# Optimization experiments

Measured on AMD Instinct MI355X. Metric: run time of the kernel, lower is better.

## Reference

```python
import jax, jax.numpy as jnp
import numpy as np

D = 64; T = 128; B = 64; R = 20; SEE = 10; H = 4; C = 4
N = 300000; P = 4000; K = 256


def setup_inputs() -> dict:
    key = jax.random.key(0)
    ks = jax.random.split(key, 24)
    g = lambda k, s: jax.random.normal(k, s, dtype=jnp.float32) * 0.05
    return {
        "prob_id": jax.random.randint(ks[0], (T, B), 0, P),
        "skills": jax.random.randint(ks[1], (T, B, C), 0, K),
        "response": jax.random.randint(ks[2], (T, B), 0, 2),
        "bg_index": jax.random.randint(ks[3], (T, B, R), 0, N),
        "mem_prob_ids": jax.random.randint(ks[4], (N,), 0, P),
        "mem_resp": jax.random.randint(ks[5], (N,), 0, 2),
        "mem_concepts": jax.random.randint(ks[6], (N, C), 0, K),
        "states_mem": g(ks[7], (N, D)),
        "concept_emb": g(ks[8], (K - 1, D)),
        "prob_emb": g(ks[9], (P - 1, D)),
        "W_pred": g(ks[10], (9 * D, 1)), "b_pred": jnp.zeros((1,), jnp.float32),
        "W_ih": g(ks[11], (4 * D, 3 * D)), "W_hh": g(ks[12], (D, 3 * D)),
        "b_ih": jnp.zeros((3 * D,), jnp.float32), "b_hh": jnp.zeros((3 * D,), jnp.float32),
        "W_batch": g(ks[13], (H, 3 * D, D)), "b_batch": jnp.zeros((H, D), jnp.float32),
        "W_bg": g(ks[14], (H, 3 * D, D)), "b_bg": jnp.zeros((H, D), jnp.float32),
        "W_bgint": g(ks[15], (6 * D, 6 * D)), "b_bgint": jnp.zeros((6 * D,), jnp.float32),
        "W_hisint": g(ks[16], (2 * D, 6 * D)), "b_hisint": jnp.zeros((6 * D,), jnp.float32),
        "W_inmap": g(ks[17], (10 * D, 4 * D)), "b_inmap": jnp.zeros((4 * D,), jnp.float32),
        "dir_w": g(ks[18], (2, 1)), "heads_map": g(ks[19], (H, 1)),
    }


def _forward(floats, ints):
    (states_mem, concept_emb, prob_emb, W_pred, b_pred, W_ih, W_hh, b_ih, b_hh,
     W_batch, b_batch, W_bg, b_bg, W_bgint, b_bgint, W_hisint, b_hisint,
     W_inmap, b_inmap, dir_w, heads_map) = floats
    prob_id, skills, response, bg_index, mem_prob_ids, mem_resp, mem_concepts = ints
    f32 = states_mem.dtype
    # embedding tables with zero row 0 (padding id)
    prob_cat = jnp.concatenate([jnp.zeros((1, D), f32), prob_emb], axis=0)
    conc_cat = jnp.concatenate([jnp.zeros((1, D), f32), concept_emb], axis=0)

    def prob_rep(pid, sk):
        pr = prob_cat[pid]                                     # [..., D]
        fsum = jnp.sum((sk != 0).astype(f32), axis=-1)
        div = jnp.where(fsum == 0, 1.0, fsum)[..., None]
        mean = jnp.sum(conc_cat[sk], axis=-2) / div            # masked-mean concept emb
        return jnp.concatenate([mean, pr], axis=-1)            # [..., 2D]

    dw = jax.nn.softmax(dir_w, axis=0)                          # [2,1]
    hm = heads_map[:, 0]                                        # [H]

    def step(carry, xt):
        h, h_buf, resp_buf, v_buf, t = carry
        pid, sk, resp, bgi = xt
        respf = resp.astype(f32)
        v = prob_rep(pid, sk)                                   # [B,2D]
        hidden_v = jnp.concatenate([h, v], axis=-1)             # [B,3D]
        bgi = bgi[:, :SEE]                                      # keep first see_ref refs
        bg_h = states_mem[bgi]                                  # [B,S,D] irregular gather
        bg_v = prob_rep(mem_prob_ids[bgi], mem_concepts[bgi])   # [B,S,2D]
        bg_r = mem_resp[bgi].astype(f32)[..., None]             # [B,S,1]
        all_hv = jnp.concatenate([bg_h, bg_v], axis=-1)         # [B,S,3D]
        bg_ctx = jnp.concatenate([all_hv * bg_r, all_hv * (1.0 - bg_r)], axis=-1)  # [B,S,6D]
        # multi-head attention over retrieved background states
        q = jnp.einsum('bk,hkd->bhd', hidden_v, W_batch) + b_batch[None]
        kk = jnp.einsum('bsk,hkd->bhsd', all_hv, W_bg) + b_bg[None, :, None, :]
        att = jax.nn.softmax(jnp.einsum('bhd,bhsd->bhs', q, kk) / np.sqrt(3.0 * D), axis=-1)
        heads = jnp.einsum('bhs,bsk->bhk', att, bg_ctx)          # [B,H,6D]
        bg_atts = jnp.einsum('bhk,h->bk', heads, hm)             # [B,6D]
        # attention over own history (positions 0..t valid)
        rb = resp_buf.astype(f32)[..., None]                     # [B,T+1,1]
        hr_cat = jnp.concatenate([h_buf * rb, h_buf * (1.0 - rb)], axis=-1)  # [B,T+1,2D]
        sc = jnp.einsum('bk,btk->bt', v, v_buf) / np.sqrt(2.0 * D)
        sc = jnp.where(jnp.arange(T + 1)[None, :] <= t, sc, -1e9)
        his_atts = jnp.einsum('bt,btk->bk', jax.nn.softmax(sc, axis=-1), hr_cat)  # [B,2D]
        peer = (bg_atts @ W_bgint + b_bgint) * dw[0, 0] + (his_atts @ W_hisint + b_hisint) * dw[1, 0]
        prob = (jnp.concatenate([peer, v, h], axis=-1) @ W_pred + b_pred)[:, 0]
        v_resp = jnp.concatenate([v * respf[:, None], v * (1.0 - respf[:, None])], axis=-1)
        gru_in = jnp.concatenate([peer, v_resp], axis=-1) @ W_inmap + b_inmap  # [B,4D]
        # GRU cell (torch GRUCell convention)
        gx = gru_in @ W_ih + b_ih
        gh = h @ W_hh + b_hh
        xr, xz, xn = jnp.split(gx, 3, axis=-1)
        hr, hz, hn = jnp.split(gh, 3, axis=-1)
        r = jax.nn.sigmoid(xr + hr)
        z = jax.nn.sigmoid(xz + hz)
        n = jnp.tanh(xn + r * hn)
        new_h = (1.0 - z) * n + z * h
        h_buf = h_buf.at[:, t + 1].set(new_h)
        resp_buf = resp_buf.at[:, t + 1].set(resp.astype(resp_buf.dtype))
        v_buf = v_buf.at[:, t + 1].set(v)
        return (new_h, h_buf, resp_buf, v_buf, t + 1), prob

    init = (jnp.zeros((B, D), f32), jnp.zeros((B, T + 1, D), f32),
            jnp.zeros((B, T + 1), jnp.int32), jnp.zeros((B, T + 1, 2 * D), f32),
            jnp.int32(0))
    xs = (prob_id, skills, response.astype(jnp.int32), bg_index)
    _, probs = jax.lax.scan(step, init, xs)                      # [T,B]
    return probs.T.reshape(-1)                                   # concat over batch, seq_num=T


def reference(prob_id, skills, response, bg_index, mem_prob_ids, mem_resp, mem_concepts,
              states_mem, concept_emb, prob_emb, W_pred, b_pred, W_ih, W_hh, b_ih, b_hh,
              W_batch, b_batch, W_bg, b_bg, W_bgint, b_bgint, W_hisint, b_hisint,
              W_inmap, b_inmap, dir_w, heads_map):
    floats = (states_mem, concept_emb, prob_emb, W_pred, b_pred, W_ih, W_hh, b_ih, b_hh,
              W_batch, b_batch, W_bg, b_bg, W_bgint, b_bgint, W_hisint, b_hisint,
              W_inmap, b_inmap, dir_w, heads_map)
    ints = (prob_id, skills, response, bg_index, mem_prob_ids, mem_resp, mem_concepts)
    return _forward(floats, ints)
```

## Files before the change

kernel.cpp:

```cpp
#include <hip/hip_runtime.h>
#include <hip/hip_bf16.h>

#define TT 128
#define BB 64
#define NITEM (TT*BB*SEE)
#define SEE 10
typedef __attribute__((ext_vector_type(8))) short short8;
typedef __attribute__((ext_vector_type(4))) float floatx4;

static __device__ __forceinline__ float wave_sum(float v) {
  v += __shfl_xor(v, 32); v += __shfl_xor(v, 16); v += __shfl_xor(v, 8);
  v += __shfl_xor(v, 4);  v += __shfl_xor(v, 2);  v += __shfl_xor(v, 1);
  return v;
}
static __device__ __forceinline__ float wave_max(float v) {
  v = fmaxf(v, __shfl_xor(v, 32)); v = fmaxf(v, __shfl_xor(v, 16)); v = fmaxf(v, __shfl_xor(v, 8));
  v = fmaxf(v, __shfl_xor(v, 4));  v = fmaxf(v, __shfl_xor(v, 2));  v = fmaxf(v, __shfl_xor(v, 1));
  return v;
}
static __device__ __forceinline__ unsigned short f2bf(float x) {
  __hip_bfloat16 h = __float2bfloat16(x);
  return *reinterpret_cast<unsigned short*>(&h);
}
static __device__ __forceinline__ float bf2f(unsigned short u) {
  unsigned v = ((unsigned)u) << 16;
  return __builtin_bit_cast(float, v);
}
static __device__ __forceinline__ unsigned int pack2(float lo, float hi) {
  return (unsigned int)f2bf(lo) | ((unsigned int)f2bf(hi) << 16);
}
static __device__ __forceinline__ void ldsbar() {
  asm volatile("s_waitcnt lgkmcnt(0)" ::: "memory");
  __builtin_amdgcn_s_barrier();
  asm volatile("" ::: "memory");
}

__global__ void build_v(const int* __restrict__ prob_id, const int* __restrict__ skills,
                        const float* __restrict__ concept_emb, const float* __restrict__ prob_emb,
                        float* __restrict__ V, float* __restrict__ VT) {
  int tb = blockIdx.x; int t = tb >> 6, b = tb & 63; int d = threadIdx.x;
  int pid = prob_id[tb];
  float pr = pid ? prob_emb[(pid - 1) * 64 + d] : 0.0f;
  int cnt = 0; float sum = 0.0f;
#pragma unroll
  for (int c = 0; c < 4; ++c) {
    int sk = skills[tb * 4 + c];
    if (sk) { ++cnt; sum += concept_emb[(sk - 1) * 64 + d]; }
  }
  float mean = sum / (float)(cnt ? cnt : 1);
  V[tb * 128 + d] = mean;
  V[tb * 128 + 64 + d] = pr;
  VT[b * 16384 + d * 128 + t] = mean;
  VT[b * 16384 + (64 + d) * 128 + t] = pr;
}

__global__ __launch_bounds__(256) void gather_ahv(
    const int* __restrict__ bg_index, const int* __restrict__ mem_prob_ids,
    const int* __restrict__ mem_concepts, const float* __restrict__ states_mem,
    const float* __restrict__ concept_emb, const float* __restrict__ prob_emb,
    unsigned short* __restrict__ AHV) {
  int gid = blockIdx.x * 256 + threadIdx.x;
  int item = gid / 96, c2 = gid - 96 * item; int d = 2 * c2;
  int t = item / 640; int rem = item - t * 640; int b = rem / 10; int s = rem - b * 10;
  int g = bg_index[(t * 64 + b) * 20 + s];
  float v0, v1;
  if (d < 64) {
    float2 sv = *(const float2*)&states_mem[g * 64 + d];
    v0 = sv.x; v1 = sv.y;
  } else if (d < 128) {
    int dd = d - 64; float s0 = 0.f, s1 = 0.f; int cnt = 0;
#pragma unroll
    for (int c = 0; c < 4; ++c) {
      int sk = mem_concepts[g * 4 + c];
      if (sk) { ++cnt; float2 e = *(const float2*)&concept_emb[(sk - 1) * 64 + dd]; s0 += e.x; s1 += e.y; }
    }
    float inv = 1.0f / (float)(cnt ? cnt : 1);
    v0 = s0 * inv; v1 = s1 * inv;
  } else {
    int dd = d - 128; int pid = mem_prob_ids[g];
    if (pid) { float2 pv = *(const float2*)&prob_emb[(pid - 1) * 64 + dd]; v0 = pv.x; v1 = pv.y; }
    else { v0 = 0.f; v1 = 0.f; }
  }
  *(unsigned int*)&AHV[(size_t)item * 192 + d] = pack2(v0, v1);
}

__global__ __launch_bounds__(256) void gemm_f32(
    const float* __restrict__ A, const float* __restrict__ B, float* __restrict__ C,
    const float* __restrict__ bias, int M, int N, int K,
    int lda, int ldb, int ldc, long sA, long sB, long sC, float scale) {
  __shared__ __align__(16) float As[64 * 36];
  __shared__ __align__(16) float Bs[32 * 64];
  const float* Ab = A + (long)blockIdx.z * sA;
  const float* Bb = B + (long)blockIdx.z * sB;
  float* Cb = C + (long)blockIdx.z * sC;
  int m0 = blockIdx.y * 64, n0 = blockIdx.x * 64;
  int tid = threadIdx.x;
  int ti = tid & 15, tj = tid >> 4;
  float acc[4][4] = {};
  for (int kc = 0; kc < K; kc += 32) {
#pragma unroll
    for (int p = 0; p < 2; ++p) {
      int q = tid + 256 * p;
      int row = q >> 3, kq = q & 7;
      *(float4*)&As[row * 36 + 4 * kq] = *(const float4*)&Ab[(size_t)(m0 + row) * lda + kc + 4 * kq];
    }
#pragma unroll
    for (int p = 0; p < 2; ++p) {
      int q = tid + 256 * p;
      int k = q >> 4, nq = q & 15;
      *(float4*)&Bs[k * 64 + 4 * nq] = *(const float4*)&Bb[(size_t)(kc + k) * ldb + n0 + 4 * nq];
    }
    __syncthreads();
#pragma unroll
    for (int k4 = 0; k4 < 8; ++k4) {
      float4 av[4], bv[4];
#pragma unroll
      for (int m = 0; m < 4; ++m) av[m] = *(const float4*)&As[(ti + 16 * m) * 36 + 4 * k4];
#pragma unroll
      for (int kk = 0; kk < 4; ++kk) bv[kk] = *(const float4*)&Bs[(4 * k4 + kk) * 64 + 4 * tj];
#pragma unroll
      for (int m = 0; m < 4; ++m) {
        const float* ap = (const float*)&av[m];
#pragma unroll
        for (int kk = 0; kk < 4; ++kk) {
          float a = ap[kk];
          acc[m][0] += a * bv[kk].x; acc[m][1] += a * bv[kk].y;
          acc[m][2] += a * bv[kk].z; acc[m][3] += a * bv[kk].w;
        }
      }
    }
    __syncthreads();
  }
  float4 bq = make_float4(0.f, 0.f, 0.f, 0.f);
  if (bias) bq = *(const float4*)&bias[n0 + 4 * tj];
#pragma unroll
  for (int m = 0; m < 4; ++m) {
    int row = m0 + ti + 16 * m;
    float4 o;
    o.x = acc[m][0] * scale + bq.x; o.y = acc[m][1] * scale + bq.y;
    o.z = acc[m][2] * scale + bq.z; o.w = acc[m][3] * scale + bq.w;
    *(float4*)&Cb[(size_t)row * ldc + n0 + 4 * tj] = o;
  }
}

__global__ __launch_bounds__(256) void k_small(
    const float* __restrict__ W_batch, const float* __restrict__ W_bg, const float* __restrict__ b_bg,
    const float* __restrict__ W_bgint, const float* __restrict__ b_bgint,
    const float* __restrict__ W_hisint, const float* __restrict__ b_hisint,
    const float* __restrict__ W_ih, const float* __restrict__ b_ih, const float* __restrict__ b_inmap,
    const float* __restrict__ W_pred, const float* __restrict__ b_pred, const float* __restrict__ dir_w,
    const float* __restrict__ b_batch,
    const float* __restrict__ M12, unsigned short* __restrict__ B1T, float* __restrict__ Hmix,
    float* __restrict__ WgT, float* __restrict__ BQG, float* __restrict__ biasQG,
    float* __restrict__ c4, float* __restrict__ cgx, float* __restrict__ uh,
    float* __restrict__ bgp, float* __restrict__ c0, float* __restrict__ dwv) {
  int idx = blockIdx.x * 256 + threadIdx.x;
  const int R0 = 49152, R1 = 86016, R2 = 122880, R3 = 147456, R4 = 196608,
            R5 = 229376, R6 = 278528, R7 = 278784, R8 = 278976, R9 = 279104,
            R10 = 279488, R11 = 279489, R12 = 279491, R13 = 280131;
  if (idx < R0) {
    int k = idx >> 8, n = idx & 255; int h = n >> 6, i = n & 63;
    float s = 0.f;
    for (int d = 0; d < 64; ++d) s += W_bg[h * 12288 + k * 64 + d] * W_batch[h * 12288 + i * 64 + d];
    B1T[n * 192 + k] = f2bf(s);
  } else if (idx < R1) {
    int r = idx - R0; int k = r / 192, c = r - k * 192;
    float s = 0.f;
    for (int j = 0; j < 384; ++j) s += W_bgint[k * 384 + j] * M12[j * 192 + c];
    B1T[(256 + c) * 192 + k] = f2bf(s);
  } else if (idx < R2) {
    int r = idx - R1; int k = r / 192, c = r - k * 192;
    float s = 0.f;
    for (int j = 0; j < 384; ++j) s += W_bgint[(192 + k) * 384 + j] * M12[j * 192 + c];
    B1T[(448 + c) * 192 + k] = f2bf(s);
  } else if (idx < R3) {
    int r = idx - R2; int i = r / 192, c = r - i * 192;
    float s = 0.f;
    for (int j = 0; j < 384; ++j) s += W_hisint[i * 384 + j] * M12[j * 192 + c];
    Hmix[i * 192 + c] = s;
  } else if (idx < R4) {
    int r = idx - R3; int h = r / 12288; int rem = r - h * 12288; int d = rem / 192, k = rem - d * 192;
    WgT[r] = W_bg[h * 12288 + k * 64 + d];
  } else if (idx < R5) {
    int r = idx - R4; int i = r >> 8, n = r & 255; int h = n >> 6, d = n & 63;
    BQG[i * 640 + n] = W_batch[h * 12288 + (64 + i) * 64 + d];
  } else if (idx < R6) {
    int r = idx - R5; int i = r / 384, c = r - i * 384;
    BQG[i * 640 + 256 + c] = (c < 192) ? M12[(384 + i) * 192 + c] : M12[(512 + i) * 192 + (c - 192)];
  } else if (idx < R7) {
    int n = idx - R6; int h = n >> 6, i = n & 63;
    float s = 0.f;
    for (int d = 0; d < 64; ++d) s += W_batch[h * 12288 + i * 64 + d] * b_bg[h * 64 + d];
    c4[n] = s;
  } else if (idx < R8) {
    int c = idx - R7;
    float e0 = __expf(dir_w[0]), e1 = __expf(dir_w[1]);
    float dw0 = e0 / (e0 + e1), dw1 = e1 / (e0 + e1);
    float s = b_ih[c];
    for (int i = 0; i < 256; ++i) s += b_inmap[i] * W_ih[i * 192 + c];
    for (int k = 0; k < 384; ++k) s += (dw0 * b_bgint[k] + dw1 * b_hisint[k]) * M12[k * 192 + c];
    cgx[c] = s;
  } else if (idx < R9) {
    int i = idx - R8;
    float s = 0.f;
    for (int j = 0; j < 384; ++j) s += W_hisint[i * 384 + j] * W_pred[j];
    uh[i] = s;
  } else if (idx < R10) {
    int k = idx - R9;
    float s = 0.f;
    for (int j = 0; j < 384; ++j) s += W_bgint[k * 384 + j] * W_pred[j];
    bgp[k] = s;
  } else if (idx < R11) {
    float e0 = __expf(dir_w[0]), e1 = __expf(dir_w[1]);
    float dw0 = e0 / (e0 + e1), dw1 = e1 / (e0 + e1);
    float s = b_pred[0];
    for (int k = 0; k < 384; ++k) s += (dw0 * b_bgint[k] + dw1 * b_hisint[k]) * W_pred[k];
    c0[0] = s;
  } else if (idx < R12) {
    float e0 = __expf(dir_w[0]), e1 = __expf(dir_w[1]);
    dwv[idx - R11] = (idx == R11) ? e0 / (e0 + e1) : e1 / (e0 + e1);
  } else if (idx < R13) {
    int i = idx - R12;
    biasQG[i] = (i < 256) ? b_batch[i] : 0.f;
  }
}

#define APAD 200
#define BPAD 40
__global__ __launch_bounds__(256) void big_gemm(
    const int* __restrict__ bg_index, const int* __restrict__ mem_resp,
    const unsigned short* __restrict__ AHV, const unsigned short* __restrict__ B1T,
    const float* __restrict__ c4, unsigned short* __restrict__ P4s16, float* __restrict__ Cg) {
  __shared__ unsigned short As[128 * APAD];
  __shared__ unsigned short Bs[128 * BPAD];
  __shared__ int rf_l[128];
  int mt = blockIdx.x;
  int tid = threadIdx.x;
  int lane = tid & 63, wv = tid >> 6;
  if (tid < 128) {
    int item = mt * 128 + tid;
    int t = item / 640; int rem = item - t * 640; int b = rem / 10; int s = rem - b * 10;
    int g = bg_index[(t * 64 + b) * 20 + s];
    rf_l[tid] = mem_resp[g];
  }
  for (int i = tid; i < 128 * 24; i += 256) {
    int row = i / 24, c = i - 24 * row;
    *(float4*)&As[row * APAD + c * 8] = *(const float4*)&AHV[(size_t)(mt * 128 + row) * 192 + c * 8];
  }
  int l15 = lane & 15, q = lane >> 4;
  int mh = (wv & 1) * 64, nh = (wv >> 1) * 64;
  const float invs192 = 0.07216878364870323f;
  for (int nt = 0; nt < 5; ++nt) {
    int n0 = nt * 128;
    floatx4 acc[4][4];
#pragma unroll
    for (int mi = 0; mi < 4; ++mi)
#pragma unroll
      for (int ni = 0; ni < 4; ++ni)
#pragma unroll
        for (int r = 0; r < 4; ++r) acc[mi][ni][r] = 0.f;
    for (int kc = 0; kc < 6; ++kc) {
      __syncthreads();
#pragma unroll
      for (int u = 0; u < 2; ++u) {
        int un = tid * 2 + u;
        int n = un >> 2, kk = (un & 3) * 8;
        *(float4*)&Bs[n * BPAD + kk] = *(const float4*)&B1T[(size_t)(n0 + n) * 192 + kc * 32 + kk];
      }
      __syncthreads();
      short8 a[4], bfr[4];
#pragma unroll
      for (int mi = 0; mi < 4; ++mi)
        a[mi] = *reinterpret_cast<const short8*>(&As[(mh + mi * 16 + l15) * APAD + kc * 32 + q * 8]);
#pragma unroll
      for (int ni = 0; ni < 4; ++ni)
        bfr[ni] = *reinterpret_cast<const short8*>(&Bs[(nh + ni * 16 + l15) * BPAD + q * 8]);
#pragma unroll
      for (int mi = 0; mi < 4; ++mi)
#pragma unroll
        for (int ni = 0; ni < 4; ++ni)
          acc[mi][ni] = __builtin_amdgcn_mfma_f32_16x16x32_bf16(a[mi], bfr[ni], acc[mi][ni], 0, 0, 0);
    }
    float c4v[4];
    if (n0 + nh < 256) {
#pragma unroll
      for (int ni = 0; ni < 4; ++ni) c4v[ni] = c4[n0 + nh + ni * 16 + l15];
    }
#pragma unroll
    for (int mi = 0; mi < 4; ++mi) {
#pragma unroll
      for (int r = 0; r < 4; ++r) {
        int row = mh + mi * 16 + q * 4 + r;
        int item = mt * 128 + row;
        int rf = rf_l[row];
#pragma unroll
        for (int ni = 0; ni < 4; ++ni) {
          int coln = n0 + nh + ni * 16 + l15;
          float o = acc[mi][ni][r];
          if (coln < 256) {
            P4s16[(size_t)item * 256 + coln] = f2bf((o + c4v[ni]) * invs192);
          } else if (coln < 448) {
            if (rf) Cg[(size_t)item * 192 + (coln - 256)] = o;
          } else {
            if (!rf) Cg[(size_t)item * 192 + (coln - 448)] = o;
          }
        }
      }
    }
  }
}

__global__ __launch_bounds__(256) void k5(
    const int* __restrict__ bg_index, const int* __restrict__ mem_resp,
    const unsigned short* __restrict__ AHV, const float* __restrict__ RQ,
    const float* __restrict__ QVG, const float* __restrict__ b_bg,
    const float* __restrict__ bgp, const float* __restrict__ V,
    const float* __restrict__ W_pred, const float* __restrict__ c0,
    float* __restrict__ SQVb, float* __restrict__ cbp, float* __restrict__ PROBC) {
  int tb = blockIdx.x;
  int tid = threadIdx.x;
  int lane = tid & 63, wv = tid >> 6;
  __shared__ float ahv[10 * 196];
  __shared__ float rql[4 * 196];
  __shared__ float bgpl[384];
  __shared__ int rf_s[10];
  __shared__ float cqb[4];
  if (tid < 10) { int g = bg_index[tb * 20 + tid]; rf_s[tid] = mem_resp[g]; }
  for (int i = tid; i < 384; i += 256) bgpl[i] = bgp[i];
  for (int i = tid; i < 768; i += 256) { int h = i / 192, c = i - h * 192; rql[h * 196 + c] = RQ[(size_t)tb * 768 + i]; }
  {
    const unsigned short* AH = &AHV[(size_t)tb * 10 * 192];
    for (int i = tid; i < 1920; i += 256) {
      int s = i / 192, c = i - 192 * s;
      ahv[s * 196 + c] = bf2f(AH[s * 192 + c]);
    }
  }
  if (tid < 4) {
    float s = 0.f;
    for (int d = 0; d < 64; ++d) s += QVG[(size_t)tb * 640 + tid * 64 + d] * b_bg[tid * 64 + d];
    cqb[tid] = s;
  }
  __syncthreads();
  const float invs192 = 0.07216878364870323f;
  for (int q = 0; q < 10; ++q) {
    float v = ahv[q * 196 + lane] * rql[wv * 196 + lane]
            + ahv[q * 196 + 64 + lane] * rql[wv * 196 + 64 + lane]
            + ahv[q * 196 + 128 + lane] * rql[wv * 196 + 128 + lane];
    v = wave_sum(v);
    if (lane == 0) SQVb[tb * 40 + wv * 10 + q] = (v + cqb[wv]) * invs192;
  }
  if (wv == 0) {
    for (int q = 0; q < 10; ++q) {
      int off = rf_s[q] ? 0 : 192;
      float v = ahv[q * 196 + lane] * bgpl[off + lane]
              + ahv[q * 196 + 64 + lane] * bgpl[off + 64 + lane]
              + ahv[q * 196 + 128 + lane] * bgpl[off + 128 + lane];
      v = wave_sum(v);
      if (lane == 0) cbp[tb * 10 + q] = v;
    }
  }
  if (wv == 1) {
    float v = V[tb * 128 + lane] * W_pred[384 + lane] + V[tb * 128 + 64 + lane] * W_pred[448 + lane];
    v = wave_sum(v);
    if (lane == 0) PROBC[tb] = v + c0[0];
  }
}

__global__ __launch_bounds__(64) void prep_pw(const float* S, const int* response,
                                              float* PW, float* PR) {
  int bt = blockIdx.x; int b = bt >> 7, t = bt & 127;
  int lane = threadIdx.x;
  size_t row = (size_t)bt * 128;
  float s0 = (lane == 0) ? 0.f : ((lane <= t) ? S[row + lane - 1] : -1e30f);
  float s1 = (lane + 64 <= t) ? S[row + lane + 63] : -1e30f;
  float m = wave_max(fmaxf(s0, s1));
  float e0 = (lane <= t) ? __expf(s0 - m) : 0.f;
  float e1 = (lane + 64 <= t) ? __expf(s1 - m) : 0.f;
  float inv = 1.f / wave_sum(e0 + e1);
  float r0 = (lane >= 1) ? (float)response[(lane - 1) * 64 + b] : 0.f;
  float r1 = (float)response[(lane + 63) * 64 + b];
  PW[row + lane] = e0 * inv;
  PW[row + 64 + lane] = e1 * inv;
  PR[row + lane] = e0 * inv * r0;
  PR[row + 64 + lane] = e1 * inv * r1;
}

__global__ __launch_bounds__(512) void seq_kernel(
    const int* __restrict__ response, const unsigned short* __restrict__ P4s16,
    const float* __restrict__ SQVb, const float* __restrict__ Cg,
    const float* __restrict__ QVG, const float* __restrict__ cbp,
    const float* __restrict__ PROBC, const float* __restrict__ PW,
    const float* __restrict__ PR, const float* __restrict__ Hmix,
    const float* __restrict__ W_hh, const float* __restrict__ b_hh,
    const float* __restrict__ cgx, const float* __restrict__ uh,
    const float* __restrict__ W_pred, const float* __restrict__ heads_map,
    const float* __restrict__ dwv, float* __restrict__ out) {
  int b = blockIdx.x;
  int tid = threadIdx.x;
  int lane = tid & 63, wv = tid >> 6;
  int cg3 = lane * 3;
  float hreg[16][3], wreg[8][3];
#pragma unroll
  for (int ii = 0; ii < 16; ++ii)
#pragma unroll
    for (int cc = 0; cc < 3; ++cc) hreg[ii][cc] = Hmix[(wv * 16 + ii) * 192 + cg3 + cc];
#pragma unroll
  for (int ii = 0; ii < 8; ++ii)
#pragma unroll
    for (int cc = 0; cc < 3; ++cc) wreg[ii][cc] = W_hh[(wv * 8 + ii) * 192 + cg3 + cc];
  float wph_reg[8], uh_reg[16];
  if (lane == 0) {
#pragma unroll
    for (int j = 0; j < 8; ++j) wph_reg[j] = W_pred[512 + wv * 8 + j];
#pragma unroll
    for (int ii = 0; ii < 16; ++ii) uh_reg[ii] = uh[wv * 16 + ii];
  }
  float bhh_reg = 0.f;
  if (tid >= 64 && tid < 256) bhh_reg = b_hh[tid - 64];
  float cgx0 = 0.f, cgx1 = 0.f, cgx2 = 0.f;
  if (tid < 64) { cgx0 = cgx[tid]; cgx1 = cgx[64 + tid]; cgx2 = cgx[128 + tid]; }
  float hmr = 0.f;
  if (tid >= 448 && tid < 452) hmr = heads_map[tid - 448];

  __shared__ float h_hist[128][64];
  __shared__ __align__(16) float PWl[128];
  __shared__ __align__(16) float PRl[128];
  __shared__ __align__(16) float h_cur[64];
  __shared__ float part_sc[8][40];
  __shared__ __align__(16) float e_l[40];
  __shared__ __align__(16) float inv_l[4];
  __shared__ __align__(16) float hisA[128];
  __shared__ float red8[8][128];
  __shared__ float redWg[8][192];
  __shared__ float redWh[8][192];
  __shared__ float gh_l[192];
  __shared__ float hwp_p[8], phis_p[8];
  __shared__ int resp_l[128];

  for (int i = tid; i < 128 * 64; i += 512) ((float*)h_hist)[i] = 0.f;
  if (tid < 64) h_cur[tid] = 0.f;
  if (tid >= 256 && tid < 384) resp_l[tid - 256] = response[(tid - 256) * 64 + b];
  float dw0 = dwv[0], dw1 = dwv[1];

  int sc_off = 0;
  if (lane < 40) { int hh = lane / 10, s = lane - hh * 10; sc_off = s * 256 + hh * 64 + wv * 8; }
  short8 pf8 = {};
  if (lane < 40) pf8 = *(const short8*)&P4s16[(size_t)b * 2560 + sc_off];
  float pf_sqv = 0.f;
  if (tid >= 384 && tid < 424) pf_sqv = SQVb[b * 40 + (tid - 384)];
  float pf_cg0[10], pf_cg1[10], pf_cg2[10];
  float pf_gxA0 = 0.f, pf_gxA1 = 0.f, pf_gxA2 = 0.f, pf_gxB0 = 0.f, pf_gxB1 = 0.f, pf_gxB2 = 0.f;
  if (tid < 64) {
#pragma unroll
    for (int s = 0; s < 10; ++s) {
      size_t base = (size_t)(b * 10 + s) * 192;
      pf_cg0[s] = Cg[base + tid]; pf_cg1[s] = Cg[base + 64 + tid]; pf_cg2[s] = Cg[base + 128 + tid];
    }
    size_t gb = (size_t)b * 640 + 256;
    pf_gxA0 = QVG[gb + tid]; pf_gxA1 = QVG[gb + 64 + tid]; pf_gxA2 = QVG[gb + 128 + tid];
    pf_gxB0 = QVG[gb + 192 + tid]; pf_gxB1 = QVG[gb + 256 + tid]; pf_gxB2 = QVG[gb + 320 + tid];
  }
  float pf_cbp[10]; float pf_probc = 0.f;
  if (tid == 448) {
#pragma unroll
    for (int s = 0; s < 10; ++s) pf_cbp[s] = cbp[b * 10 + s];
    pf_probc = PROBC[b];
  }
  float4 pf_pw = make_float4(0, 0, 0, 0), pf_pr = pf_pw;
  if (tid >= 128 && tid < 160) pf_pw = *(const float4*)&PW[((size_t)(b * 128 + 0)) * 128 + 4 * (tid - 128)];
  else if (tid >= 160 && tid < 192) pf_pr = *(const float4*)&PR[((size_t)(b * 128 + 0)) * 128 + 4 * (tid - 160)];
  if (tid >= 128 && tid < 160) *(float4*)&PWl[4 * (tid - 128)] = pf_pw;
  else if (tid >= 160 && tid < 192) *(float4*)&PRl[4 * (tid - 160)] = pf_pr;
  if (tid >= 128 && tid < 160) pf_pw = *(const float4*)&PW[((size_t)(b * 128 + 1)) * 128 + 4 * (tid - 128)];
  else if (tid >= 160 && tid < 192) pf_pr = *(const float4*)&PR[((size_t)(b * 128 + 1)) * 128 + 4 * (tid - 160)];
  ldsbar();

  for (int t = 0; t < 128; ++t) {
    int tn = (t < 127) ? t + 1 : 127;
    int tbn = tn * 64 + b;
    float4 ha = *(const float4*)&h_cur[wv * 8];
    float4 hb = *(const float4*)&h_cur[wv * 8 + 4];
    if (lane < 40) {
      const unsigned short* pp = (const unsigned short*)&pf8;
      float v = ha.x * bf2f(pp[0]) + ha.y * bf2f(pp[1]) + ha.z * bf2f(pp[2]) + ha.w * bf2f(pp[3])
              + hb.x * bf2f(pp[4]) + hb.y * bf2f(pp[5]) + hb.z * bf2f(pp[6]) + hb.w * bf2f(pp[7]);
      part_sc[wv][lane] = v;
      pf8 = *(const short8*)&P4s16[(size_t)tbn * 2560 + sc_off];
    }
    {
      float hl[8] = {ha.x, ha.y, ha.z, ha.w, hb.x, hb.y, hb.z, hb.w};
      float l0 = 0.f, l1 = 0.f, l2 = 0.f;
#pragma unroll
      for (int ii = 0; ii < 8; ++ii) {
        l0 += hl[ii] * wreg[ii][0]; l1 += hl[ii] * wreg[ii][1]; l2 += hl[ii] * wreg[ii][2];
      }
      redWg[wv][cg3] = l0; redWg[wv][cg3 + 1] = l1; redWg[wv][cg3 + 2] = l2;
      if (lane == 0) {
        float hp = 0.f;
#pragma unroll
        for (int j = 0; j < 8; ++j) hp += hl[j] * wph_reg[j];
        hwp_p[wv] = hp;
      }
    }
    {
      int j0 = wv * 16;
      float aR = 0.f, aA = 0.f;
#pragma unroll
      for (int k = 0; k < 16; ++k) {
        float hv = h_hist[j0 + k][lane];
        aA += PWl[j0 + k] * hv; aR += PRl[j0 + k] * hv;
      }
      red8[wv][lane] = aR; red8[wv][64 + lane] = aA;
    }
    ldsbar();
    if (tid < 64) {
      float sR = 0.f, sA = 0.f;
#pragma unroll
      for (int g = 0; g < 8; ++g) { sR += red8[g][tid]; sA += red8[g][64 + tid]; }
      hisA[tid] = sR; hisA[64 + tid] = sA - sR;
    } else if (tid < 256) {
      int c = tid - 64; float g = 0.f;
#pragma unroll
      for (int gg = 0; gg < 8; ++gg) g += redWg[gg][c];
      gh_l[c] = g + bhh_reg;
    } else if (tid >= 384 && tid < 424) {
      int p = tid - 384;
      float s = pf_sqv;
#pragma unroll
      for (int w = 0; w < 8; ++w) s += part_sc[w][p];
      e_l[p] = __expf(s);
      pf_sqv = SQVb[tbn * 40 + p];
    }
    ldsbar();
    {
      float4 h0 = *(const float4*)&hisA[wv * 16];
      float4 h1 = *(const float4*)&hisA[wv * 16 + 4];
      float4 h2 = *(const float4*)&hisA[wv * 16 + 8];
      float4 h3 = *(const float4*)&hisA[wv * 16 + 12];
      float hA[16] = {h0.x, h0.y, h0.z, h0.w, h1.x, h1.y, h1.z, h1.w,
                      h2.x, h2.y, h2.z, h2.w, h3.x, h3.y, h3.z, h3.w};
      float l0 = 0.f, l1 = 0.f, l2 = 0.f;
#pragma unroll
      for (int ii = 0; ii < 16; ++ii) {
        l0 += hA[ii] * hreg[ii][0]; l1 += hA[ii] * hreg[ii][1]; l2 += hA[ii] * hreg[ii][2];
      }
      redWh[wv][cg3] = l0; redWh[wv][cg3 + 1] = l1; redWh[wv][cg3 + 2] = l2;
      if (lane == 0) {
        float pp = 0.f;
#pragma unroll
        for (int ii = 0; ii < 16; ++ii) pp += hA[ii] * uh_reg[ii];
        phis_p[wv] = pp;
      }
    }
    if (tid >= 448 && tid < 452) {
      int h = tid - 448;
      float den = 0.f;
#pragma unroll
      for (int s = 0; s < 10; ++s) den += e_l[h * 10 + s];
      inv_l[h] = hmr / den;
    }
    ldsbar();
    if (tid < 64 || tid == 448) {
      float4 iv = *(const float4*)&inv_l[0];
      float ev[40];
#pragma unroll
      for (int qq = 0; qq < 10; ++qq) *(float4*)&ev[4 * qq] = *(const float4*)&e_l[4 * qq];
      float ws[10];
#pragma unroll
      for (int s = 0; s < 10; ++s)
        ws[s] = iv.x * ev[s] + iv.y * ev[10 + s] + iv.z * ev[20 + s] + iv.w * ev[30 + s];
      if (tid < 64) {
        float gxh0 = 0.f, gxh1 = 0.f, gxh2 = 0.f;
#pragma unroll
        for (int g = 0; g < 8; ++g) {
          gxh0 += redWh[g][tid]; gxh1 += redWh[g][64 + tid]; gxh2 += redWh[g][128 + tid];
        }
        float gbg0 = 0.f, gbg1 = 0.f, gbg2 = 0.f;
#pragma unroll
        for (int s = 0; s < 10; ++s) {
          gbg0 += ws[s] * pf_cg0[s]; gbg1 += ws[s] * pf_cg1[s]; gbg2 += ws[s] * pf_cg2[s];
        }
        int rn = resp_l[t];
        float xr = dw0 * gbg0 + dw1 * gxh0 + (rn ? pf_gxA0 : pf_gxB0) + cgx0;
        float xz = dw0 * gbg1 + dw1 * gxh1 + (rn ? pf_gxA1 : pf_gxB1) + cgx1;
        float xn = dw0 * gbg2 + dw1 * gxh2 + (rn ? pf_gxA2 : pf_gxB2) + cgx2;
        float hr = gh_l[tid], hz = gh_l[64 + tid], hn = gh_l[128 + tid];
        float r = 1.f / (1.f + __expf(-(xr + hr)));
        float z = 1.f / (1.f + __expf(-(xz + hz)));
        float n = tanhf(xn + r * hn);
        float hnew = (1.f - z) * n + z * h_cur[tid];
        h_cur[tid] = hnew;
        if (t < 127) h_hist[t + 1][tid] = hnew;
#pragma unroll
        for (int s = 0; s < 10; ++s) {
          size_t base = (size_t)(tbn * 10 + s) * 192;
          pf_cg0[s] = Cg[base + tid]; pf_cg1[s] = Cg[base + 64 + tid]; pf_cg2[s] = Cg[base + 128 + tid];
        }
        size_t gb = (size_t)tbn * 640 + 256;
        pf_gxA0 = QVG[gb + tid]; pf_gxA1 = QVG[gb + 64 + tid]; pf_gxA2 = QVG[gb + 128 + tid];
        pf_gxB0 = QVG[gb + 192 + tid]; pf_gxB1 = QVG[gb + 256 + tid]; pf_gxB2 = QVG[gb + 320 + tid];
      } else {
        float pbg = 0.f;
#pragma unroll
        for (int s = 0; s < 10; ++s) pbg += ws[s] * pf_cbp[s];
        float ph = 0.f, hw = 0.f;
#pragma unroll
        for (int g = 0; g < 8; ++g) { ph += phis_p[g]; hw += hwp_p[g]; }
        out[b * 128 + t] = dw0 * pbg + dw1 * ph + hw + pf_probc;
#pragma unroll
        for (int s = 0; s < 10; ++s) pf_cbp[s] = cbp[tbn * 10 + s];
        pf_probc = PROBC[tbn];
      }
    } else if (tid >= 128 && tid < 192) {
      if (tid < 160) *(float4*)&PWl[4 * (tid - 128)] = pf_pw;
      else *(float4*)&PRl[4 * (tid - 160)] = pf_pr;
      int rn2 = (t + 2 < 128) ? t + 2 : 127;
      if (tid < 160) pf_pw = *(const float4*)&PW[((size_t)(b * 128 + rn2)) * 128 + 4 * (tid - 128)];
      else pf_pr = *(const float4*)&PR[((size_t)(b * 128 + rn2)) * 128 + 4 * (tid - 160)];
    }
    ldsbar();
  }
}

extern "C" void kernel_launch(void* const* d_in, const int* in_sizes, int n_in,
                              void* d_out, int out_size, void* d_ws, size_t ws_size,
                              hipStream_t stream) {
  const int* prob_id      = (const int*)d_in[0];
  const int* skills       = (const int*)d_in[1];
  const int* response     = (const int*)d_in[2];
  const int* bg_index     = (const int*)d_in[3];
  const int* mem_prob_ids = (const int*)d_in[4];
  const int* mem_resp     = (const int*)d_in[5];
  const int* mem_concepts = (const int*)d_in[6];
  const float* states_mem  = (const float*)d_in[7];
  const float* concept_emb = (const float*)d_in[8];
  const float* prob_emb    = (const float*)d_in[9];
  const float* W_pred   = (const float*)d_in[10];
  const float* b_pred   = (const float*)d_in[11];
  const float* W_ih     = (const float*)d_in[12];
  const float* W_hh     = (const float*)d_in[13];
  const float* b_ih     = (const float*)d_in[14];
  const float* b_hh     = (const float*)d_in[15];
  const float* W_batch  = (const float*)d_in[16];
  const float* b_batch  = (const float*)d_in[17];
  const float* W_bg     = (const float*)d_in[18];
  const float* b_bg     = (const float*)d_in[19];
  const float* W_bgint  = (const float*)d_in[20];
  const float* b_bgint  = (const float*)d_in[21];
  const float* W_hisint = (const float*)d_in[22];
  const float* b_hisint = (const float*)d_in[23];
  const float* W_inmap  = (const float*)d_in[24];
  const float* b_inmap  = (const float*)d_in[25];
  const float* dir_w    = (const float*)d_in[26];
  const float* heads_map= (const float*)d_in[27];
  float* out = (float*)d_out;

  float* w = (float*)d_ws;
  size_t off = 0;
  auto alloc = [&](size_t n) { float* p = w + off; off += (n + 3) & ~(size_t)3; return p; };
  float* M12    = alloc(640 * 192);
  unsigned short* B1T = (unsigned short*)alloc(640 * 192 / 2);
  float* Hmix   = alloc(128 * 192);
  float* WgT    = alloc(4 * 192 * 64);
  float* BQG    = alloc(128 * 640);
  float* biasQG = alloc(640);
  float* c4     = alloc(256);
  float* cgx    = alloc(192);
  float* uh     = alloc(128);
  float* bgp    = alloc(384);
  float* c0     = alloc(1);
  float* dwv    = alloc(2);
  float* V      = alloc((size_t)8192 * 128);
  float* VT     = alloc((size_t)64 * 128 * 128);
  float* QVG    = alloc((size_t)8192 * 640);
  float* RQ     = alloc((size_t)8192 * 768);
  float* S      = alloc((size_t)64 * 128 * 128);
  float* PR     = alloc((size_t)64 * 128 * 128);
  unsigned short* AHV = (unsigned short*)alloc((size_t)NITEM * 192 / 2);
  unsigned short* P4s16 = (unsigned short*)alloc((size_t)NITEM * 256 / 2);
  float* Cg     = alloc((size_t)NITEM * 192);
  float* SQVb   = alloc((size_t)8192 * 40);
  float* cbp    = alloc((size_t)NITEM);
  float* PROBC  = alloc(8192);
  (void)ws_size; (void)in_sizes; (void)n_in; (void)out_size;

  build_v<<<8192, 64, 0, stream>>>(prob_id, skills, concept_emb, prob_emb, V, VT);
  gather_ahv<<<NITEM * 96 / 256, 256, 0, stream>>>(bg_index, mem_prob_ids, mem_concepts,
      states_mem, concept_emb, prob_emb, AHV);
  gemm_f32<<<dim3(3, 10, 1), 256, 0, stream>>>(W_inmap, W_ih, M12, nullptr,
      640, 192, 256, 256, 192, 192, 0, 0, 0, 1.0f);
  k_small<<<1095, 256, 0, stream>>>(W_batch, W_bg, b_bg, W_bgint, b_bgint, W_hisint, b_hisint,
      W_ih, b_ih, b_inmap, W_pred, b_pred, dir_w, b_batch, M12, B1T, Hmix, WgT, BQG, biasQG,
      c4, cgx, uh, bgp, c0, dwv);
  gemm_f32<<<dim3(10, 128, 1), 256, 0, stream>>>(V, BQG, QVG, biasQG,
      8192, 640, 128, 128, 640, 640, 0, 0, 0, 1.0f);
  gemm_f32<<<dim3(3, 128, 4), 256, 0, stream>>>(QVG, WgT, RQ, nullptr,
      8192, 192, 64, 640, 192, 768, 64, 12288, 192, 1.0f);
  gemm_f32<<<dim3(2, 2, 64), 256, 0, stream>>>(V, VT, S, nullptr,
      128, 128, 128, 8192, 128, 128, 128, 16384, 16384, 0.08838834764831845f);
  prep_pw<<<8192, 64, 0, stream>>>(S, response, S, PR);
  big_gemm<<<dim3(640), 256, 0, stream>>>(bg_index, mem_resp, AHV, B1T, c4, P4s16, Cg);
  k5<<<8192, 256, 0, stream>>>(bg_index, mem_resp, AHV, RQ, QVG, b_bg, bgp, V, W_pred, c0,
      SQVb, cbp, PROBC);
  seq_kernel<<<64, 512, 0, stream>>>(response, P4s16, SQVb, Cg, QVG, cbp, PROBC,
      S, PR, Hmix, W_hh, b_hh, cgx, uh, W_pred, heads_map, dwv, out);
}
```

Baseline: 762.9 us.

## Split big_gemm N-tiles across grid and shrink seq_kernel to four waves

big_gemm now launches one block per (M-tile, N-tile) instead of looping over five N-tiles inside each block. This gives more parallelism, at the cost of reloading the A tile five times. seq_kernel drops from 8 to 4 waves per block, so each wave handles twice as many hidden rows in registers. The aim is to shorten the per-step barrier and cross-wave reduction cost in the sequential recurrence. The trade-off is more registers and more serial work per thread.

```diff
diff --git a/kernel.cpp b/kernel.cpp
--- a/kernel.cpp
+++ b/kernel.cpp
@@ -235,6 +235,8 @@
   __shared__ unsigned short Bs[128 * BPAD];
   __shared__ int rf_l[128];
   int mt = blockIdx.x;
+  int nt = blockIdx.y;
+  int n0 = nt * 128;
   int tid = threadIdx.x;
   int lane = tid & 63, wv = tid >> 6;
   if (tid < 128) {
@@ -250,60 +252,57 @@
   int l15 = lane & 15, q = lane >> 4;
   int mh = (wv & 1) * 64, nh = (wv >> 1) * 64;
   const float invs192 = 0.07216878364870323f;
-  for (int nt = 0; nt < 5; ++nt) {
-    int n0 = nt * 128;
-    floatx4 acc[4][4];
+  floatx4 acc[4][4];
+#pragma unroll
+  for (int mi = 0; mi < 4; ++mi)
+#pragma unroll
+    for (int ni = 0; ni < 4; ++ni)
+#pragma unroll
+      for (int r = 0; r < 4; ++r) acc[mi][ni][r] = 0.f;
+  for (int kc = 0; kc < 6; ++kc) {
+    __syncthreads();
+#pragma unroll
+    for (int u = 0; u < 2; ++u) {
+      int un = tid * 2 + u;
+      int n = un >> 2, kk = (un & 3) * 8;
+      *(float4*)&Bs[n * BPAD + kk] = *(const float4*)&B1T[(size_t)(n0 + n) * 192 + kc * 32 + kk];
+    }
+    __syncthreads();
+    short8 a[4], bfr[4];
 #pragma unroll
     for (int mi = 0; mi < 4; ++mi)
+      a[mi] = *reinterpret_cast<const short8*>(&As[(mh + mi * 16 + l15) * APAD + kc * 32 + q * 8]);
+#pragma unroll
+    for (int ni = 0; ni < 4; ++ni)
+      bfr[ni] = *reinterpret_cast<const short8*>(&Bs[(nh + ni * 16 + l15) * BPAD + q * 8]);
+#pragma unroll
+    for (int mi = 0; mi < 4; ++mi)
 #pragma unroll
       for (int ni = 0; ni < 4; ++ni)
-#pragma unroll
-        for (int r = 0; r < 4; ++r) acc[mi][ni][r] = 0.f;
-    for (int kc = 0; kc < 6; ++kc) {
-      __syncthreads();
-#pragma unroll
-      for (int u = 0; u < 2; ++u) {
-        int un = tid * 2 + u;
-        int n = un >> 2, kk = (un & 3) * 8;
-        *(float4*)&Bs[n * BPAD + kk] = *(const float4*)&B1T[(size_t)(n0 + n) * 192 + kc * 32 + kk];
-      }
-      __syncthreads();
-      short8 a[4], bfr[4];
-#pragma unroll
-      for (int mi = 0; mi < 4; ++mi)
-        a[mi] = *reinterpret_cast<const short8*>(&As[(mh + mi * 16 + l15) * APAD + kc * 32 + q * 8]);
-#pragma unroll
-      for (int ni = 0; ni < 4; ++ni)
-        bfr[ni] = *reinterpret_cast<const short8*>(&Bs[(nh + ni * 16 + l15) * BPAD + q * 8]);
-#pragma unroll
-      for (int mi = 0; mi < 4; ++mi)
-#pragma unroll
-        for (int ni = 0; ni < 4; ++ni)
-          acc[mi][ni] = __builtin_amdgcn_mfma_f32_16x16x32_bf16(a[mi], bfr[ni], acc[mi][ni], 0, 0, 0);
-    }
-    float c4v[4];
-    if (n0 + nh < 256) {
-#pragma unroll
-      for (int ni = 0; ni < 4; ++ni) c4v[ni] = c4[n0 + nh + ni * 16 + l15];
-    }
-#pragma unroll
-    for (int mi = 0; mi < 4; ++mi) {
-#pragma unroll
-      for (int r = 0; r < 4; ++r) {
-        int row = mh + mi * 16 + q * 4 + r;
-        int item = mt * 128 + row;
-        int rf = rf_l[row];
-#pragma unroll
-        for (int ni = 0; ni < 4; ++ni) {
-          int coln = n0 + nh + ni * 16 + l15;
-          float o = acc[mi][ni][r];
-          if (coln < 256) {
-            P4s16[(size_t)item * 256 + coln] = f2bf((o + c4v[ni]) * invs192);
-          } else if (coln < 448) {
-            if (rf) Cg[(size_t)item * 192 + (coln - 256)] = o;
-          } else {
-            if (!rf) Cg[(size_t)item * 192 + (coln - 448)] = o;
-          }
+        acc[mi][ni] = __builtin_amdgcn_mfma_f32_16x16x32_bf16(a[mi], bfr[ni], acc[mi][ni], 0, 0, 0);
+  }
+  float c4v[4];
+  if (n0 + nh < 256) {
+#pragma unroll
+    for (int ni = 0; ni < 4; ++ni) c4v[ni] = c4[n0 + nh + ni * 16 + l15];
+  }
+#pragma unroll
+  for (int mi = 0; mi < 4; ++mi) {
+#pragma unroll
+    for (int r = 0; r < 4; ++r) {
+      int row = mh + mi * 16 + q * 4 + r;
+      int item = mt * 128 + row;
+      int rf = rf_l[row];
+#pragma unroll
+      for (int ni = 0; ni < 4; ++ni) {
+        int coln = n0 + nh + ni * 16 + l15;
+        float o = acc[mi][ni][r];
+        if (coln < 256) {
+          P4s16[(size_t)item * 256 + coln] = f2bf((o + c4v[ni]) * invs192);
+        } else if (coln < 448) {
+          if (rf) Cg[(size_t)item * 192 + (coln - 256)] = o;
+        } else {
+          if (!rf) Cg[(size_t)item * 192 + (coln - 448)] = o;
         }
       }
     }
@@ -385,7 +384,7 @@
   PR[row + 64 + lane] = e1 * inv * r1;
 }
 
-__global__ __launch_bounds__(512) void seq_kernel(
+__global__ __launch_bounds__(256) void seq_kernel(
     const int* __restrict__ response, const unsigned short* __restrict__ P4s16,
     const float* __restrict__ SQVb, const float* __restrict__ Cg,
     const float* __restrict__ QVG, const float* __restrict__ cbp,
@@ -399,55 +398,59 @@
   int tid = threadIdx.x;
   int lane = tid & 63, wv = tid >> 6;
   int cg3 = lane * 3;
-  float hreg[16][3], wreg[8][3];
+  float hreg[32][3], wreg[16][3];
+#pragma unroll
+  for (int ii = 0; ii < 32; ++ii)
+#pragma unroll
+    for (int cc = 0; cc < 3; ++cc) hreg[ii][cc] = Hmix[(wv * 32 + ii) * 192 + cg3 + cc];
 #pragma unroll
   for (int ii = 0; ii < 16; ++ii)
 #pragma unroll
-    for (int cc = 0; cc < 3; ++cc) hreg[ii][cc] = Hmix[(wv * 16 + ii) * 192 + cg3 + cc];
-#pragma unroll
-  for (int ii = 0; ii < 8; ++ii)
-#pragma unroll
-    for (int cc = 0; cc < 3; ++cc) wreg[ii][cc] = W_hh[(wv * 8 + ii) * 192 + cg3 + cc];
-  float wph_reg[8], uh_reg[16];
+    for (int cc = 0; cc < 3; ++cc) wreg[ii][cc] = W_hh[(wv * 16 + ii) * 192 + cg3 + cc];
+  float wph_reg[16], uh_reg[32];
   if (lane == 0) {
 #pragma unroll
-    for (int j = 0; j < 8; ++j) wph_reg[j] = W_pred[512 + wv * 8 + j];
-#pragma unroll
-    for (int ii = 0; ii < 16; ++ii) uh_reg[ii] = uh[wv * 16 + ii];
-  }
-  float bhh_reg = 0.f;
-  if (tid >= 64 && tid < 256) bhh_reg = b_hh[tid - 64];
+    for (int j = 0; j < 16; ++j) wph_reg[j] = W_pred[512 + wv * 16 + j];
+#pragma unroll
+    for (int ii = 0; ii < 32; ++ii) uh_reg[ii] = uh[wv * 32 + ii];
+  }
+  float bhh0 = 0.f, bhh1 = 0.f, bhh2 = 0.f;
+  if (tid >= 64) bhh0 = b_hh[tid - 64];
   float cgx0 = 0.f, cgx1 = 0.f, cgx2 = 0.f;
   if (tid < 64) { cgx0 = cgx[tid]; cgx1 = cgx[64 + tid]; cgx2 = cgx[128 + tid]; }
+  (void)bhh1; (void)bhh2;
   float hmr = 0.f;
-  if (tid >= 448 && tid < 452) hmr = heads_map[tid - 448];
+  if (tid >= 100 && tid < 104) hmr = heads_map[tid - 100];
 
   __shared__ float h_hist[128][64];
   __shared__ __align__(16) float PWl[128];
   __shared__ __align__(16) float PRl[128];
   __shared__ __align__(16) float h_cur[64];
-  __shared__ float part_sc[8][40];
+  __shared__ float part_sc[4][40];
   __shared__ __align__(16) float e_l[40];
   __shared__ __align__(16) float inv_l[4];
   __shared__ __align__(16) float hisA[128];
-  __shared__ float red8[8][128];
-  __shared__ float redWg[8][192];
-  __shared__ float redWh[8][192];
+  __shared__ float red8[4][128];
+  __shared__ float redWg[4][192];
+  __shared__ float redWh[4][192];
   __shared__ float gh_l[192];
-  __shared__ float hwp_p[8], phis_p[8];
+  __shared__ float hwp_p[4], phis_p[4];
   __shared__ int resp_l[128];
 
-  for (int i = tid; i < 128 * 64; i += 512) ((float*)h_hist)[i] = 0.f;
+  for (int i = tid; i < 128 * 64; i += 256) ((float*)h_hist)[i] = 0.f;
   if (tid < 64) h_cur[tid] = 0.f;
-  if (tid >= 256 && tid < 384) resp_l[tid - 256] = response[(tid - 256) * 64 + b];
+  if (tid >= 128) resp_l[tid - 128] = response[(tid - 128) * 64 + b];
   float dw0 = dwv[0], dw1 = dwv[1];
 
   int sc_off = 0;
-  if (lane < 40) { int hh = lane / 10, s = lane - hh * 10; sc_off = s * 256 + hh * 64 + wv * 8; }
-  short8 pf8 = {};
-  if (lane < 40) pf8 = *(const short8*)&P4s16[(size_t)b * 2560 + sc_off];
+  if (lane < 40) { int hh = lane / 10, s = lane - hh * 10; sc_off = s * 256 + hh * 64 + wv * 16; }
+  short8 pf8a = {}, pf8b = {};
+  if (lane < 40) {
+    pf8a = *(const short8*)&P4s16[(size_t)b * 2560 + sc_off];
+    pf8b = *(const short8*)&P4s16[(size_t)b * 2560 + sc_off + 8];
+  }
   float pf_sqv = 0.f;
-  if (tid >= 384 && tid < 424) pf_sqv = SQVb[b * 40 + (tid - 384)];
+  if (tid >= 216) pf_sqv = SQVb[b * 40 + (tid - 216)];
   float pf_cg0[10], pf_cg1[10], pf_cg2[10];
   float pf_gxA0 = 0.f, pf_gxA1 = 0.f, pf_gxA2 = 0.f, pf_gxB0 = 0.f, pf_gxB1 = 0.f, pf_gxB2 = 0.f;
   if (tid < 64) {
@@ -461,7 +464,7 @@
     pf_gxB0 = QVG[gb + 192 + tid]; pf_gxB1 = QVG[gb + 256 + tid]; pf_gxB2 = QVG[gb + 320 + tid];
   }
   float pf_cbp[10]; float pf_probc = 0.f;
-  if (tid == 448) {
+  if (tid == 192) {
 #pragma unroll
     for (int s = 0; s < 10; ++s) pf_cbp[s] = cbp[b * 10 + s];
     pf_probc = PROBC[b];
@@ -478,35 +481,43 @@
   for (int t = 0; t < 128; ++t) {
     int tn = (t < 127) ? t + 1 : 127;
     int tbn = tn * 64 + b;
-    float4 ha = *(const float4*)&h_cur[wv * 8];
-    float4 hb = *(const float4*)&h_cur[wv * 8 + 4];
+    float4 ha = *(const float4*)&h_cur[wv * 16];
+    float4 hb = *(const float4*)&h_cur[wv * 16 + 4];
+    float4 hc4 = *(const float4*)&h_cur[wv * 16 + 8];
+    float4 hd = *(const float4*)&h_cur[wv * 16 + 12];
+    float hl[16] = {ha.x, ha.y, ha.z, ha.w, hb.x, hb.y, hb.z, hb.w,
+                    hc4.x, hc4.y, hc4.z, hc4.w, hd.x, hd.y, hd.z, hd.w};
     if (lane < 40) {
-      const unsigned short* pp = (const unsigned short*)&pf8;
-      float v = ha.x * bf2f(pp[0]) + ha.y * bf2f(pp[1]) + ha.z * bf2f(pp[2]) + ha.w * bf2f(pp[3])
-              + hb.x * bf2f(pp[4]) + hb.y * bf2f(pp[5]) + hb.z * bf2f(pp[6]) + hb.w * bf2f(pp[7]);
+      const unsigned short* p1 = (const unsigned short*)&pf8a;
+      const unsigned short* p2 = (const unsigned short*)&pf8b;
+      float v = 0.f;
+#pragma unroll
+      for (int j = 0; j < 8; ++j) v += hl[j] * bf2f(p1[j]);
+#pragma unroll
+      for (int j = 0; j < 8; ++j) v += hl[8 + j] * bf2f(p2[j]);
       part_sc[wv][lane] = v;
-      pf8 = *(const short8*)&P4s16[(size_t)tbn * 2560 + sc_off];
+      pf8a = *(const short8*)&P4s16[(size_t)tbn * 2560 + sc_off];
+      pf8b = *(const short8*)&P4s16[(size_t)tbn * 2560 + sc_off + 8];
     }
     {
-      float hl[8] = {ha.x, ha.y, ha.z, ha.w, hb.x, hb.y, hb.z, hb.w};
       float l0 = 0.f, l1 = 0.f, l2 = 0.f;
 #pragma unroll
-      for (int ii = 0; ii < 8; ++ii) {
+      for (int ii = 0; ii < 16; ++ii) {
         l0 += hl[ii] * wreg[ii][0]; l1 += hl[ii] * wreg[ii][1]; l2 += hl[ii] * wreg[ii][2];
       }
       redWg[wv][cg3] = l0; redWg[wv][cg3 + 1] = l1; redWg[wv][cg3 + 2] = l2;
       if (lane == 0) {
         float hp = 0.f;
 #pragma unroll
-        for (int j = 0; j < 8; ++j) hp += hl[j] * wph_reg[j];
+        for (int j = 0; j < 16; ++j) hp += hl[j] * wph_reg[j];
         hwp_p[wv] = hp;
       }
     }
     {
-      int j0 = wv * 16;
+      int j0 = wv * 32;
       float aR = 0.f, aA = 0.f;
 #pragma unroll
-      for (int k = 0; k < 16; ++k) {
+      for (int k = 0; k < 32; ++k) {
         float hv = h_hist[j0 + k][lane];
         aA += PWl[j0 + k] * hv; aR += PRl[j0 + k] * hv;
       }
@@ -514,53 +525,47 @@
     }
     ldsbar();
     if (tid < 64) {
-      float sR = 0.f, sA = 0.f;
-#pragma unroll
-      for (int g = 0; g < 8; ++g) { sR += red8[g][tid]; sA += red8[g][64 + tid]; }
+      float sR = red8[0][tid] + red8[1][tid] + red8[2][tid] + red8[3][tid];
+      float sA = red8[0][64 + tid] + red8[1][64 + tid] + red8[2][64 + tid] + red8[3][64 + tid];
       hisA[tid] = sR; hisA[64 + tid] = sA - sR;
-    } else if (tid < 256) {
-      int c = tid - 64; float g = 0.f;
-#pragma unroll
-      for (int gg = 0; gg < 8; ++gg) g += redWg[gg][c];
-      gh_l[c] = g + bhh_reg;
-    } else if (tid >= 384 && tid < 424) {
-      int p = tid - 384;
-      float s = pf_sqv;
-#pragma unroll
-      for (int w = 0; w < 8; ++w) s += part_sc[w][p];
-      e_l[p] = __expf(s);
-      pf_sqv = SQVb[tbn * 40 + p];
+    } else {
+      int c = tid - 64;
+      float g = redWg[0][c] + redWg[1][c] + redWg[2][c] + redWg[3][c];
+      gh_l[c] = g + bhh0;
+      if (tid >= 216) {
+        int p = tid - 216;
+        float s = pf_sqv + part_sc[0][p] + part_sc[1][p] + part_sc[2][p] + part_sc[3][p];
+        e_l[p] = __expf(s);
+        pf_sqv = SQVb[tbn * 40 + p];
+      }
     }
     ldsbar();
     {
-      float4 h0 = *(const float4*)&hisA[wv * 16];
-      float4 h1 = *(const float4*)&hisA[wv * 16 + 4];
-      float4 h2 = *(const float4*)&hisA[wv * 16 + 8];
-      float4 h3 = *(const float4*)&hisA[wv * 16 + 12];
-      float hA[16] = {h0.x, h0.y, h0.z, h0.w, h1.x, h1.y, h1.z, h1.w,
-                      h2.x, h2.y, h2.z, h2.w, h3.x, h3.y, h3.z, h3.w};
+      float hA[32];
+#pragma unroll
+      for (int k = 0; k < 8; ++k) *(float4*)&hA[4 * k] = *(const float4*)&hisA[wv * 32 + 4 * k];
       float l0 = 0.f, l1 = 0.f, l2 = 0.f;
 #pragma unroll
-      for (int ii = 0; ii < 16; ++ii) {
+      for (int ii = 0; ii < 32; ++ii) {
         l0 += hA[ii] * hreg[ii][0]; l1 += hA[ii] * hreg[ii][1]; l2 += hA[ii] * hreg[ii][2];
       }
       redWh[wv][cg3] = l0; redWh[wv][cg3 + 1] = l1; redWh[wv][cg3 + 2] = l2;
       if (lane == 0) {
         float pp = 0.f;
 #pragma unroll
-        for (int ii = 0; ii < 16; ++ii) pp += hA[ii] * uh_reg[ii];
+        for (int ii = 0; ii < 32; ++ii) pp += hA[ii] * uh_reg[ii];
         phis_p[wv] = pp;
       }
     }
-    if (tid >= 448 && tid < 452) {
-      int h = tid - 448;
+    if (tid >= 100 && tid < 104) {
+      int h = tid - 100;
       float den = 0.f;
 #pragma unroll
       for (int s = 0; s < 10; ++s) den += e_l[h * 10 + s];
       inv_l[h] = hmr / den;
     }
     ldsbar();
-    if (tid < 64 || tid == 448) {
+    if (tid < 64 || tid == 192) {
       float4 iv = *(const float4*)&inv_l[0];
       float ev[40];
 #pragma unroll
@@ -570,11 +575,9 @@
       for (int s = 0; s < 10; ++s)
         ws[s] = iv.x * ev[s] + iv.y * ev[10 + s] + iv.z * ev[20 + s] + iv.w * ev[30 + s];
       if (tid < 64) {
-        float gxh0 = 0.f, gxh1 = 0.f, gxh2 = 0.f;
-#pragma unroll
-        for (int g = 0; g < 8; ++g) {
-          gxh0 += redWh[g][tid]; gxh1 += redWh[g][64 + tid]; gxh2 += redWh[g][128 + tid];
-        }
+        float gxh0 = redWh[0][tid] + redWh[1][tid] + redWh[2][tid] + redWh[3][tid];
+        float gxh1 = redWh[0][64 + tid] + redWh[1][64 + tid] + redWh[2][64 + tid] + redWh[3][64 + tid];
+        float gxh2 = redWh[0][128 + tid] + redWh[1][128 + tid] + redWh[2][128 + tid] + redWh[3][128 + tid];
         float gbg0 = 0.f, gbg1 = 0.f, gbg2 = 0.f;
 #pragma unroll
         for (int s = 0; s < 10; ++s) {
@@ -603,9 +606,8 @@
         float pbg = 0.f;
 #pragma unroll
         for (int s = 0; s < 10; ++s) pbg += ws[s] * pf_cbp[s];
-        float ph = 0.f, hw = 0.f;
-#pragma unroll
-        for (int g = 0; g < 8; ++g) { ph += phis_p[g]; hw += hwp_p[g]; }
+        float ph = phis_p[0] + phis_p[1] + phis_p[2] + phis_p[3];
+        float hw = hwp_p[0] + hwp_p[1] + hwp_p[2] + hwp_p[3];
         out[b * 128 + t] = dw0 * pbg + dw1 * ph + hw + pf_probc;
 #pragma unroll
         for (int s = 0; s < 10; ++s) pf_cbp[s] = cbp[tbn * 10 + s];
@@ -699,9 +701,9 @@
   gemm_f32<<<dim3(2, 2, 64), 256, 0, stream>>>(V, VT, S, nullptr,
       128, 128, 128, 8192, 128, 128, 128, 16384, 16384, 0.08838834764831845f);
   prep_pw<<<8192, 64, 0, stream>>>(S, response, S, PR);
-  big_gemm<<<dim3(640), 256, 0, stream>>>(bg_index, mem_resp, AHV, B1T, c4, P4s16, Cg);
+  big_gemm<<<dim3(640, 5), 256, 0, stream>>>(bg_index, mem_resp, AHV, B1T, c4, P4s16, Cg);
   k5<<<8192, 256, 0, stream>>>(bg_index, mem_resp, AHV, RQ, QVG, b_bg, bgp, V, W_pred, c0,
       SQVb, cbp, PROBC);
-  seq_kernel<<<64, 512, 0, stream>>>(response, P4s16, SQVb, Cg, QVG, cbp, PROBC,
+  seq_kernel<<<64, 256, 0, stream>>>(response, P4s16, SQVb, Cg, QVG, cbp, PROBC,
       S, PR, Hmix, W_hh, b_hh, cgx, uh, W_pred, heads_map, dwv, out);
 }
```

New measurement: 889.3 us. 1.17x slower.
